# Kernel optimization log

Hardware: AMD Instinct MI355X
Metric: run time of the kernel (lower is better)

## Reference

```python
import jax, jax.numpy as jnp
import numpy as np

N, D, H = 2048, 128, 40


def setup_inputs() -> dict:
    key = jax.random.key(0)
    kx, kw, kv = jax.random.split(key, 3)
    X = jax.random.normal(kx, (N, D), dtype=jnp.float32)
    # nn.Parameter(torch.randn(D, D) / D) per head, stacked over H
    W = jax.random.normal(kw, (H, D, D), dtype=jnp.float32) / D
    V = jax.random.normal(kv, (H, D, D), dtype=jnp.float32) / D
    return {"X": X, "W": W, "V": V}


def reference(X, W, V):
    d = X.shape[1]
    # scores[h] = X @ W[h] @ X.T / sqrt(D)   -> [H, N, N]
    XW = jnp.einsum("nd,hde->hne", X, W)
    scores = jnp.einsum("hne,me->hnm", XW, X) / jnp.sqrt(jnp.asarray(d, X.dtype))
    # softmax over dim=1 of the 2D per-head score matrix == last axis here
    weights = jax.nn.softmax(scores, axis=-1) + 1e-8
    # A[h] = weights[h] @ X @ V[h]; output = sum over heads -> [N, D]
    XV = jnp.einsum("md,hde->hme", X, V)
    out = jnp.einsum("hnm,hme->ne", weights, XV)
    return out
```

## Files before the change

kernel.cpp:

```cpp
#include <hip/hip_runtime.h>
#include <hip/hip_bf16.h>
#include <stdint.h>

#define N 2048
#define D 128
#define H 40

typedef __attribute__((ext_vector_type(8))) short short8;
typedef __attribute__((ext_vector_type(4))) float float4v;
typedef __attribute__((ext_vector_type(8))) float float8v;
typedef __attribute__((ext_vector_type(16))) float float16v;
typedef __attribute__((ext_vector_type(8))) _Float16 half8v;

static __device__ __forceinline__ unsigned short f32_to_bf16(float f) {
  unsigned int u = __builtin_bit_cast(unsigned int, f);
  unsigned int rounding = 0x7FFFu + ((u >> 16) & 1u);
  return (unsigned short)((u + rounding) >> 16);
}

static __device__ __forceinline__ unsigned int pk2(float lo, float hi) {
  return (unsigned int)f32_to_bf16(lo) | ((unsigned int)f32_to_bf16(hi) << 16);
}

static __device__ __forceinline__ unsigned int pk2f(float lo, float hi) {
  unsigned int a = __builtin_bit_cast(unsigned int, lo) + 0x8000u;
  unsigned int b = __builtin_bit_cast(unsigned int, hi) + 0x8000u;
  return __builtin_amdgcn_perm(b, a, 0x07060302u);
}

static __device__ __forceinline__ unsigned long long pack4(float x0, float x1,
                                                           float x2, float x3) {
  return (unsigned long long)pk2(x0, x1) | ((unsigned long long)pk2(x2, x3) << 32);
}

static __device__ __forceinline__ float fast_exp2(float x) {
#if __has_builtin(__builtin_amdgcn_exp2f)
  return __builtin_amdgcn_exp2f(x);
#else
  return __expf(0.69314718056f * x);
#endif
}

static __device__ __forceinline__ void load_lds16(const void* g, void* l) {
  __builtin_amdgcn_global_load_lds(
      (const __attribute__((address_space(1))) unsigned int*)g,
      (__attribute__((address_space(3))) unsigned int*)l, 16, 0, 0);
}

#define MFMA32(a, b, c) __builtin_amdgcn_mfma_f32_32x32x16_bf16((a), (b), (c), 0, 0, 0)

static __device__ __forceinline__ void regs_to_bfrags(const float16v c, int hh,
                                                      short8& f0, short8& f1) {
  unsigned int a0 = pk2f(c[0], c[1]),   a1 = pk2f(c[2], c[3]);
  unsigned int a2 = pk2f(c[4], c[5]),   a3 = pk2f(c[6], c[7]);
  unsigned int a4 = pk2f(c[8], c[9]),   a5 = pk2f(c[10], c[11]);
  unsigned int a6 = pk2f(c[12], c[13]), a7 = pk2f(c[14], c[15]);
  unsigned int x0 = __shfl_xor(hh ? a0 : a2, 32);
  unsigned int x1 = __shfl_xor(hh ? a1 : a3, 32);
  unsigned int x2 = __shfl_xor(hh ? a4 : a6, 32);
  unsigned int x3 = __shfl_xor(hh ? a5 : a7, 32);
  uint4 u0 = {hh ? x0 : a0, hh ? x1 : a1, hh ? a2 : x0, hh ? a3 : x1};
  uint4 u1 = {hh ? x2 : a4, hh ? x3 : a5, hh ? a6 : x2, hh ? a7 : x3};
  f0 = __builtin_bit_cast(short8, u0);
  f1 = __builtin_bit_cast(short8, u1);
}

static __device__ __forceinline__ void regs_to_pfrags(const float16v s, int hh,
                                                      float& lsum, short8& f0,
                                                      short8& f1) {
  float e[16];
  float acc = 0.0f;
#pragma unroll
  for (int i = 0; i < 16; i++) { e[i] = fast_exp2(s[i]); acc += e[i]; }
  lsum += acc;
  unsigned int a0 = pk2f(e[0], e[1]),   a1 = pk2f(e[2], e[3]);
  unsigned int a2 = pk2f(e[4], e[5]),   a3 = pk2f(e[6], e[7]);
  unsigned int a4 = pk2f(e[8], e[9]),   a5 = pk2f(e[10], e[11]);
  unsigned int a6 = pk2f(e[12], e[13]), a7 = pk2f(e[14], e[15]);
  unsigned int x0 = __shfl_xor(hh ? a0 : a2, 32);
  unsigned int x1 = __shfl_xor(hh ? a1 : a3, 32);
  unsigned int x2 = __shfl_xor(hh ? a4 : a6, 32);
  unsigned int x3 = __shfl_xor(hh ? a5 : a7, 32);
  uint4 u0 = {hh ? x0 : a0, hh ? x1 : a1, hh ? a2 : x0, hh ? a3 : x1};
  uint4 u1 = {hh ? x2 : a4, hh ? x3 : a5, hh ? a6 : x2, hh ? a7 : x3};
  f0 = __builtin_bit_cast(short8, u0);
  f1 = __builtin_bit_cast(short8, u1);
}

static __device__ __forceinline__ void stage_64x256(const char* gbase, size_t stride,
                                                    int colOff, char* lds, int wave,
                                                    int lane) {
#pragma unroll
  for (int i = 0; i < 4; i++) {
    int r = wave * 16 + i * 4 + (lane >> 4);
    int us = (lane & 15) ^ (r & 15);
    load_lds16(gbase + (size_t)r * stride + colOff + us * 16,
               lds + (wave * 16 + i * 4) * 256);
  }
}
static __device__ __forceinline__ void stage_128x256(const char* gbase, size_t stride,
                                                     char* lds, int wave, int lane) {
#pragma unroll
  for (int i = 0; i < 8; i++) {
    int r = wave * 32 + i * 4 + (lane >> 4);
    int us = (lane & 15) ^ (r & 15);
    load_lds16(gbase + (size_t)r * stride + us * 16, lds + (wave * 32 + i * 4) * 256);
  }
}
static __device__ __forceinline__ void stage_128x128(const char* gbase, size_t stride,
                                                     int colOff, char* lds, int wave,
                                                     int lane) {
#pragma unroll
  for (int i = 0; i < 4; i++) {
    int m = wave * 16 + i * 4 + (lane >> 4);
    int u = (lane & 15) ^ (m & 15);
    int grow = 2 * m + (u >> 3);
    load_lds16(gbase + (size_t)grow * stride + colOff + (u & 7) * 16,
               lds + (wave * 16 + i * 4) * 256);
  }
}
static __device__ __forceinline__ short8 read_macro(const char* lds, int row, int kunit) {
  int m = row >> 1;
  int u = ((row & 1) << 3) | kunit;
  return *(const short8*)(lds + m * 256 + ((u ^ (m & 15)) * 16));
}

__global__ __launch_bounds__(256)
void xconv_kernel(const float* __restrict__ X, unsigned short* __restrict__ Xb,
                  unsigned short* __restrict__ XbT) {
  const int n0 = blockIdx.x * 128;
  const int tid = threadIdx.x;
  __shared__ __align__(16) unsigned short Lt[128 * 136];
  for (int i = tid; i < 128 * 32; i += 256) {
    int row = i >> 5, c4 = (i & 31) * 4;
    float4v x = *(const float4v*)(X + (size_t)(n0 + row) * D + c4);
    unsigned long long p = pack4(x.x, x.y, x.z, x.w);
    *(unsigned long long*)(Lt + row * 136 + c4) = p;
    *(unsigned long long*)(Xb + (size_t)(n0 + row) * D + c4) = p;
  }
  __syncthreads();
  for (int i = tid; i < 128 * 16; i += 256) {
    int d = i >> 4, g = i & 15;
    short8 v;
#pragma unroll
    for (int j = 0; j < 8; j++) v[j] = (short)Lt[(g * 8 + j) * 136 + d];
    *(short8*)(XbT + (size_t)d * N + n0 + g * 8) = v;
  }
}

__global__ __launch_bounds__(256)
void wvconv_kernel(const float* __restrict__ W, const float* __restrict__ V,
                   unsigned short* __restrict__ Wt, unsigned short* __restrict__ Vt) {
  const int b = blockIdx.x;
  const int mat = (b >= H) ? 1 : 0;
  const int h = mat ? b - H : b;
  const float* src = (mat ? V : W) + (size_t)h * D * D;
  unsigned short* dst = (mat ? Vt : Wt) + (size_t)h * D * D;
  const float scale = mat ? 1.0f : 0.1275174313f;
  const int tid = threadIdx.x;
  __shared__ __align__(16) unsigned short Lt[128 * 136];
  for (int i = tid; i < 128 * 32; i += 256) {
    int d = i >> 5, e4 = (i & 31) * 4;
    float4v w = *(const float4v*)(src + d * D + e4);
    Lt[(e4 + 0) * 136 + d] = f32_to_bf16(w.x * scale);
    Lt[(e4 + 1) * 136 + d] = f32_to_bf16(w.y * scale);
    Lt[(e4 + 2) * 136 + d] = f32_to_bf16(w.z * scale);
    Lt[(e4 + 3) * 136 + d] = f32_to_bf16(w.w * scale);
  }
  __syncthreads();
  for (int i = tid; i < 128 * 16; i += 256) {
    int e = i >> 4, u = i & 15;
    *(uint4*)((char*)dst + (size_t)e * 256 + u * 16) =
        *(const uint4*)((const char*)Lt + (size_t)e * 272 + u * 16);
  }
}

__global__ __launch_bounds__(256)
void attn_kernel(const unsigned short* __restrict__ Xb,
                 const unsigned short* __restrict__ XbT,
                 const unsigned short* __restrict__ Wt,
                 const unsigned short* __restrict__ Vt,
                 unsigned short* __restrict__ Opart, float* __restrict__ Lsum) {
  __shared__ __align__(16) char smem[32768];
  const int bx = blockIdx.x;
  const int kh = bx & 1;
  const int q0 = ((bx >> 1) & 15) << 7;
  const int h = bx >> 5;
  const int tid = threadIdx.x;
  const int wave = tid >> 6, lane = tid & 63;
  const int l = lane & 31, hh = lane >> 5;

  const char* XbB = (const char*)Xb;
  const char* XbTB = (const char*)XbT;
  const char* WtB = (const char*)(Wt + (size_t)h * D * D);
  const char* VtB = (const char*)(Vt + (size_t)h * D * D);

  float16v qa[4];
#pragma unroll
  for (int et = 0; et < 4; et++) qa[et] = (float16v)0.0f;
#pragma unroll
  for (int dh = 0; dh < 2; dh++) {
    __syncthreads();
    stage_128x128(XbB + (size_t)q0 * 256, 256, dh * 128, smem, wave, lane);
    stage_128x128(WtB, 256, dh * 128, smem + 16384, wave, lane);
    __syncthreads();
    short8 xfr[4];
#pragma unroll
    for (int dk = 0; dk < 4; dk++)
      xfr[dk] = read_macro(smem, wave * 32 + l, dk * 2 + hh);
#pragma unroll
    for (int et = 0; et < 4; et++)
#pragma unroll
      for (int dk = 0; dk < 4; dk++) {
        short8 wa = read_macro(smem + 16384, et * 32 + l, dk * 2 + hh);
        qa[et] = MFMA32(wa, xfr[dk], qa[et]);
      }
  }
  short8 qf[8];
#pragma unroll
  for (int et = 0; et < 4; et++)
    regs_to_bfrags(qa[et], hh, qf[2 * et], qf[2 * et + 1]);

  float16v Tacc[4];
#pragma unroll
  for (int dt = 0; dt < 4; dt++) Tacc[dt] = (float16v)0.0f;
  float lsum = 0.0f;

  const int kbase = kh * (N / 2);
  for (int kt = 0; kt < 16; kt++) {
    const int k0 = kbase + kt * 64;
    __syncthreads();
    stage_64x256(XbB + (size_t)k0 * 256, 256, 0, smem, wave, lane);
    stage_128x128(XbTB, 4096, k0 * 2, smem + 16384, wave, lane);
    __syncthreads();
#pragma unroll
    for (int ksub = 0; ksub < 2; ksub++) {
      float16v sa = (float16v)0.0f, sb = (float16v)0.0f;
      const int krow = ksub * 32 + l;
#pragma unroll
      for (int ks = 0; ks < 4; ks++) {
        short8 kfa = *(const short8*)(smem + krow * 256 +
                                      (((2 * ks + hh) ^ (krow & 15)) * 16));
        short8 kfb = *(const short8*)(smem + krow * 256 +
                                      (((2 * (ks + 4) + hh) ^ (krow & 15)) * 16));
        sa = MFMA32(kfa, qf[ks], sa);
        sb = MFMA32(kfb, qf[ks + 4], sb);
      }
      float16v s = sa + sb;
      short8 pf0, pf1;
      regs_to_pfrags(s, hh, lsum, pf0, pf1);
#pragma unroll
      for (int kk = 0; kk < 2; kk++) {
        short8 pf = kk ? pf1 : pf0;
#pragma unroll
        for (int dt = 0; dt < 4; dt++) {
          short8 xt = read_macro(smem + 16384, dt * 32 + l, ksub * 4 + kk * 2 + hh);
          Tacc[dt] = MFMA32(xt, pf, Tacc[dt]);
        }
      }
    }
  }

  float tot = lsum + __shfl_xor(lsum, 32);
  if (hh == 0) Lsum[(size_t)(h * 2 + kh) * N + q0 + wave * 32 + l] = tot;

  short8 tb[8];
#pragma unroll
  for (int dt = 0; dt < 4; dt++)
    regs_to_bfrags(Tacc[dt], hh, tb[2 * dt], tb[2 * dt + 1]);

  __syncthreads();
  stage_128x256(VtB, 256, smem, wave, lane);
  __syncthreads();

  float16v oacc[4];
#pragma unroll
  for (int et = 0; et < 4; et++) oacc[et] = (float16v)0.0f;
#pragma unroll
  for (int et = 0; et < 4; et++) {
    const int erow = et * 32 + l;
#pragma unroll
    for (int dk = 0; dk < 8; dk++) {
      short8 va = *(const short8*)(smem + erow * 256 +
                                   (((2 * dk + hh) ^ (erow & 15)) * 16));
      oacc[et] = MFMA32(va, tb[dk], oacc[et]);
    }
  }

  unsigned short* Oph = Opart + (size_t)(h * 2 + kh) * N * D;
#pragma unroll
  for (int pass = 0; pass < 2; pass++) {
    __syncthreads();
    const int qrow = wave * 32 + l;
#pragma unroll
    for (int etL = 0; etL < 2; etL++) {
      int et = pass * 2 + etL;
#pragma unroll
      for (int g = 0; g < 4; g++) {
        int unit = etL * 8 + 2 * g + hh;
        float4v v;
        v.x = oacc[et][4 * g + 0];
        v.y = oacc[et][4 * g + 1];
        v.z = oacc[et][4 * g + 2];
        v.w = oacc[et][4 * g + 3];
        *(float4v*)(smem + qrow * 256 + ((unit ^ (qrow & 15)) * 16)) = v;
      }
    }
    __syncthreads();
#pragma unroll
    for (int i = 0; i < 8; i++) {
      int idx = i * 256 + tid;
      int qr = idx >> 4, up = idx & 15, u = up ^ (qr & 15);
      float4v v = *(const float4v*)(smem + qr * 256 + up * 16);
      auto h0 = __builtin_amdgcn_cvt_pkrtz(v.x, v.y);
      auto h1 = __builtin_amdgcn_cvt_pkrtz(v.z, v.w);
      uint2 st = {__builtin_bit_cast(unsigned int, h0),
                  __builtin_bit_cast(unsigned int, h1)};
      *(uint2*)(Oph + (size_t)(q0 + qr) * D + pass * 64 + u * 4) = st;
    }
  }
}

__global__ __launch_bounds__(256)
void reduce_kernel(const unsigned short* __restrict__ Opart,
                   const float* __restrict__ Lsum, float* __restrict__ out) {
  int idx = blockIdx.x * 256 + threadIdx.x;
  int n = idx >> 4;
  const uint4* base = (const uint4*)Opart;
  float8v acc = (float8v)0.0f;
#pragma unroll 4
  for (int h = 0; h < H; h++) {
    float lt = Lsum[(size_t)(2 * h) * N + n] + Lsum[(size_t)(2 * h + 1) * N + n];
    float il = __builtin_amdgcn_rcpf(lt);
    uint4 a = base[(size_t)(2 * h) * (N * D / 8) + idx];
    uint4 b = base[(size_t)(2 * h + 1) * (N * D / 8) + idx];
    float8v fa = __builtin_convertvector(__builtin_bit_cast(half8v, a), float8v);
    float8v fb = __builtin_convertvector(__builtin_bit_cast(half8v, b), float8v);
    acc += (fa + fb) * il;
  }
  *(float8v*)(out + (size_t)idx * 8) = acc;
}

extern "C" void kernel_launch(void* const* d_in, const int* in_sizes, int n_in,
                              void* d_out, int out_size, void* d_ws, size_t ws_size,
                              hipStream_t stream) {
  const float* X = (const float*)d_in[0];
  const float* W = (const float*)d_in[1];
  const float* V = (const float*)d_in[2];
  float* out = (float*)d_out;

  unsigned short* Xb = (unsigned short*)d_ws;
  unsigned short* XbT = Xb + (size_t)N * D;
  unsigned short* Wt = XbT + (size_t)N * D;
  unsigned short* Vt = Wt + (size_t)H * D * D;
  unsigned short* Opart = Vt + (size_t)H * D * D;
  float* Lsum = (float*)(Opart + (size_t)H * 2 * N * D);

  xconv_kernel<<<dim3(N / 128), 256, 0, stream>>>(X, Xb, XbT);
  wvconv_kernel<<<dim3(2 * H), 256, 0, stream>>>(W, V, Wt, Vt);
  attn_kernel<<<dim3(16 * 2 * H), 256, 0, stream>>>(Xb, XbT, Wt, Vt, Opart, Lsum);
  reduce_kernel<<<dim3(N * D / 8 / 256), 256, 0, stream>>>(Opart, Lsum, out);
}
```

Baseline: 224.4 us.

## Use FP8 MFMA for scores, double-buffer K tiles, fuse prep kernels

Computes the QK score MFMA in FP8. The query projection is scaled by 64 and X is converted to FP8, and the scale is undone inside exp2. The K/X^T tiles are double-buffered in LDS so the next tile loads while the current one computes, and the V tile staging overlaps the final loop iteration. It also merges the two conversion kernels into one launch, loads the X fragments for the projection directly from global memory, and widens the reduce grid. FP8 scores risk extra precision loss in the softmax, and the larger LDS footprint may reduce occupancy.

```diff
diff --git a/kernel.cpp b/kernel.cpp
--- a/kernel.cpp
+++ b/kernel.cpp
@@ -5,12 +5,12 @@
 #define N 2048
 #define D 128
 #define H 40
+#define NT 16
 
 typedef __attribute__((ext_vector_type(8))) short short8;
 typedef __attribute__((ext_vector_type(4))) float float4v;
-typedef __attribute__((ext_vector_type(8))) float float8v;
 typedef __attribute__((ext_vector_type(16))) float float16v;
-typedef __attribute__((ext_vector_type(8))) _Float16 half8v;
+typedef __attribute__((ext_vector_type(4))) _Float16 half4v;
 
 static __device__ __forceinline__ unsigned short f32_to_bf16(float f) {
   unsigned int u = __builtin_bit_cast(unsigned int, f);
@@ -41,6 +41,15 @@
 #endif
 }
 
+static __device__ __forceinline__ float bf2f(unsigned short u) {
+  unsigned int x = ((unsigned int)u) << 16;
+  return __builtin_bit_cast(float, x);
+}
+
+static __device__ __forceinline__ long long mk64(unsigned int lo, unsigned int hi) {
+  return (long long)(((unsigned long long)hi << 32) | lo);
+}
+
 static __device__ __forceinline__ void load_lds16(const void* g, void* l) {
   __builtin_amdgcn_global_load_lds(
       (const __attribute__((address_space(1))) unsigned int*)g,
@@ -48,6 +57,7 @@
 }
 
 #define MFMA32(a, b, c) __builtin_amdgcn_mfma_f32_32x32x16_bf16((a), (b), (c), 0, 0, 0)
+#define MFMA8(a, b, c) __builtin_amdgcn_mfma_f32_32x32x16_fp8_fp8((a), (b), (c), 0, 0, 0)
 
 static __device__ __forceinline__ void regs_to_bfrags(const float16v c, int hh,
                                                       short8& f0, short8& f1) {
@@ -65,13 +75,30 @@
   f1 = __builtin_bit_cast(short8, u1);
 }
 
+static __device__ __forceinline__ void regs_to_f8frags(const float16v c, int hh,
+                                                       long long& f0, long long& f1) {
+  const float s = 64.0f;
+  int v0 = __builtin_amdgcn_cvt_pk_fp8_f32(c[0] * s, c[1] * s, 0, false);
+  v0 = __builtin_amdgcn_cvt_pk_fp8_f32(c[2] * s, c[3] * s, v0, true);
+  int v1 = __builtin_amdgcn_cvt_pk_fp8_f32(c[4] * s, c[5] * s, 0, false);
+  v1 = __builtin_amdgcn_cvt_pk_fp8_f32(c[6] * s, c[7] * s, v1, true);
+  int v2 = __builtin_amdgcn_cvt_pk_fp8_f32(c[8] * s, c[9] * s, 0, false);
+  v2 = __builtin_amdgcn_cvt_pk_fp8_f32(c[10] * s, c[11] * s, v2, true);
+  int v3 = __builtin_amdgcn_cvt_pk_fp8_f32(c[12] * s, c[13] * s, 0, false);
+  v3 = __builtin_amdgcn_cvt_pk_fp8_f32(c[14] * s, c[15] * s, v3, true);
+  int t0 = __shfl_xor(hh ? v0 : v1, 32);
+  int t1 = __shfl_xor(hh ? v2 : v3, 32);
+  f0 = hh ? mk64((unsigned)t0, (unsigned)v1) : mk64((unsigned)v0, (unsigned)t0);
+  f1 = hh ? mk64((unsigned)t1, (unsigned)v3) : mk64((unsigned)v2, (unsigned)t1);
+}
+
 static __device__ __forceinline__ void regs_to_pfrags(const float16v s, int hh,
                                                       float& lsum, short8& f0,
                                                       short8& f1) {
   float e[16];
   float acc = 0.0f;
 #pragma unroll
-  for (int i = 0; i < 16; i++) { e[i] = fast_exp2(s[i]); acc += e[i]; }
+  for (int i = 0; i < 16; i++) { e[i] = fast_exp2(s[i] * 0.015625f); acc += e[i]; }
   lsum += acc;
   unsigned int a0 = pk2f(e[0], e[1]),   a1 = pk2f(e[2], e[3]);
   unsigned int a2 = pk2f(e[4], e[5]),   a3 = pk2f(e[6], e[7]);
@@ -119,6 +146,17 @@
                lds + (wave * 16 + i * 4) * 256);
   }
 }
+static __device__ __forceinline__ void stage_k8(const char* gbase, char* lds,
+                                                int wave, int lane) {
+#pragma unroll
+  for (int i = 0; i < 2; i++) {
+    int m = wave * 8 + i * 4 + (lane >> 4);
+    int u = (lane & 15) ^ (m & 15);
+    int grow = 2 * m + (u >> 3);
+    load_lds16(gbase + (size_t)grow * 128 + (u & 7) * 16,
+               lds + (wave * 8 + i * 4) * 256);
+  }
+}
 static __device__ __forceinline__ short8 read_macro(const char* lds, int row, int kunit) {
   int m = row >> 1;
   int u = ((row & 1) << 3) | kunit;
@@ -126,62 +164,82 @@
 }
 
 __global__ __launch_bounds__(256)
-void xconv_kernel(const float* __restrict__ X, unsigned short* __restrict__ Xb,
-                  unsigned short* __restrict__ XbT) {
-  const int n0 = blockIdx.x * 128;
+void prep_kernel(const float* __restrict__ X, const float* __restrict__ W,
+                 const float* __restrict__ V, unsigned short* __restrict__ Xb,
+                 unsigned short* __restrict__ XbT, unsigned char* __restrict__ Xf8,
+                 unsigned short* __restrict__ Wt, unsigned short* __restrict__ Vt) {
   const int tid = threadIdx.x;
   __shared__ __align__(16) unsigned short Lt[128 * 136];
-  for (int i = tid; i < 128 * 32; i += 256) {
-    int row = i >> 5, c4 = (i & 31) * 4;
-    float4v x = *(const float4v*)(X + (size_t)(n0 + row) * D + c4);
-    unsigned long long p = pack4(x.x, x.y, x.z, x.w);
-    *(unsigned long long*)(Lt + row * 136 + c4) = p;
-    *(unsigned long long*)(Xb + (size_t)(n0 + row) * D + c4) = p;
-  }
-  __syncthreads();
-  for (int i = tid; i < 128 * 16; i += 256) {
-    int d = i >> 4, g = i & 15;
-    short8 v;
-#pragma unroll
-    for (int j = 0; j < 8; j++) v[j] = (short)Lt[(g * 8 + j) * 136 + d];
-    *(short8*)(XbT + (size_t)d * N + n0 + g * 8) = v;
-  }
-}
-
-__global__ __launch_bounds__(256)
-void wvconv_kernel(const float* __restrict__ W, const float* __restrict__ V,
-                   unsigned short* __restrict__ Wt, unsigned short* __restrict__ Vt) {
-  const int b = blockIdx.x;
-  const int mat = (b >= H) ? 1 : 0;
-  const int h = mat ? b - H : b;
-  const float* src = (mat ? V : W) + (size_t)h * D * D;
-  unsigned short* dst = (mat ? Vt : Wt) + (size_t)h * D * D;
-  const float scale = mat ? 1.0f : 0.1275174313f;
-  const int tid = threadIdx.x;
-  __shared__ __align__(16) unsigned short Lt[128 * 136];
-  for (int i = tid; i < 128 * 32; i += 256) {
-    int d = i >> 5, e4 = (i & 31) * 4;
-    float4v w = *(const float4v*)(src + d * D + e4);
-    Lt[(e4 + 0) * 136 + d] = f32_to_bf16(w.x * scale);
-    Lt[(e4 + 1) * 136 + d] = f32_to_bf16(w.y * scale);
-    Lt[(e4 + 2) * 136 + d] = f32_to_bf16(w.z * scale);
-    Lt[(e4 + 3) * 136 + d] = f32_to_bf16(w.w * scale);
-  }
-  __syncthreads();
-  for (int i = tid; i < 128 * 16; i += 256) {
-    int e = i >> 4, u = i & 15;
-    *(uint4*)((char*)dst + (size_t)e * 256 + u * 16) =
-        *(const uint4*)((const char*)Lt + (size_t)e * 272 + u * 16);
+  if (blockIdx.x < 16) {
+    const int n0 = blockIdx.x * 128;
+    for (int i = tid; i < 128 * 32; i += 256) {
+      int row = i >> 5, c4 = (i & 31) * 4;
+      float4v x = *(const float4v*)(X + (size_t)(n0 + row) * D + c4);
+      unsigned long long p = pack4(x.x, x.y, x.z, x.w);
+      *(unsigned long long*)(Lt + row * 136 + c4) = p;
+      *(unsigned long long*)(Xb + (size_t)(n0 + row) * D + c4) = p;
+    }
+    __syncthreads();
+    for (int i = tid; i < 128 * 16; i += 256) {
+      int d = i >> 4, g = i & 15;
+      short8 v;
+#pragma unroll
+      for (int j = 0; j < 8; j++) v[j] = (short)Lt[(g * 8 + j) * 136 + d];
+      *(short8*)(XbT + (size_t)d * N + n0 + g * 8) = v;
+    }
+    for (int i = tid; i < 128 * 8; i += 256) {
+      int row = i >> 3, c = i & 7, t = c >> 1, o8 = (c & 1) * 8;
+      const unsigned short* lp = Lt + row * 136;
+      int d0 = t * 32 + o8, d1 = t * 32 + 16 + o8;
+      short8 xa = *(const short8*)(lp + d0);
+      short8 xb = *(const short8*)(lp + d1);
+      int w0 = __builtin_amdgcn_cvt_pk_fp8_f32(bf2f(xa[0]), bf2f(xa[1]), 0, false);
+      w0 = __builtin_amdgcn_cvt_pk_fp8_f32(bf2f(xa[2]), bf2f(xa[3]), w0, true);
+      int w1 = __builtin_amdgcn_cvt_pk_fp8_f32(bf2f(xa[4]), bf2f(xa[5]), 0, false);
+      w1 = __builtin_amdgcn_cvt_pk_fp8_f32(bf2f(xa[6]), bf2f(xa[7]), w1, true);
+      int w2 = __builtin_amdgcn_cvt_pk_fp8_f32(bf2f(xb[0]), bf2f(xb[1]), 0, false);
+      w2 = __builtin_amdgcn_cvt_pk_fp8_f32(bf2f(xb[2]), bf2f(xb[3]), w2, true);
+      int w3 = __builtin_amdgcn_cvt_pk_fp8_f32(bf2f(xb[4]), bf2f(xb[5]), 0, false);
+      w3 = __builtin_amdgcn_cvt_pk_fp8_f32(bf2f(xb[6]), bf2f(xb[7]), w3, true);
+      uint4 st = {(unsigned)w0, (unsigned)w1, (unsigned)w2, (unsigned)w3};
+      *(uint4*)(Xf8 + (size_t)(n0 + row) * 128 + c * 16) = st;
+    }
+  } else {
+    const int b = blockIdx.x - 16;
+    const int mat = (b >= H) ? 1 : 0;
+    const int h = mat ? b - H : b;
+    const float* src = (mat ? V : W) + (size_t)h * D * D;
+    unsigned short* dst = (mat ? Vt : Wt) + (size_t)h * D * D;
+    const float scale = mat ? 1.0f : 0.1275174313f;
+    for (int i = tid; i < 128 * 32; i += 256) {
+      int d = i >> 5, e4 = (i & 31) * 4;
+      float4v w = *(const float4v*)(src + d * D + e4);
+      Lt[(e4 + 0) * 136 + d] = f32_to_bf16(w.x * scale);
+      Lt[(e4 + 1) * 136 + d] = f32_to_bf16(w.y * scale);
+      Lt[(e4 + 2) * 136 + d] = f32_to_bf16(w.z * scale);
+      Lt[(e4 + 3) * 136 + d] = f32_to_bf16(w.w * scale);
+    }
+    __syncthreads();
+    for (int i = tid; i < 128 * 16; i += 256) {
+      int e = i >> 4, u = i & 15;
+      *(uint4*)((char*)dst + (size_t)e * 256 + u * 16) =
+          *(const uint4*)((const char*)Lt + (size_t)e * 272 + u * 16);
+    }
   }
 }
 
 __global__ __launch_bounds__(256)
 void attn_kernel(const unsigned short* __restrict__ Xb,
+                 const unsigned char* __restrict__ Xf8,
                  const unsigned short* __restrict__ XbT,
                  const unsigned short* __restrict__ Wt,
                  const unsigned short* __restrict__ Vt,
                  unsigned short* __restrict__ Opart, float* __restrict__ Lsum) {
-  __shared__ __align__(16) char smem[32768];
+  __shared__ __align__(16) char smem[49152];
+  char* XA = smem;
+  char* XB = smem + 16384;
+  char* KA = smem + 32768;
+  char* KB = smem + 40960;
   const int bx = blockIdx.x;
   const int kh = bx & 1;
   const int q0 = ((bx >> 1) & 15) << 7;
@@ -191,62 +249,71 @@
   const int l = lane & 31, hh = lane >> 5;
 
   const char* XbB = (const char*)Xb;
+  const char* Xf8B = (const char*)Xf8;
   const char* XbTB = (const char*)XbT;
   const char* WtB = (const char*)(Wt + (size_t)h * D * D);
   const char* VtB = (const char*)(Vt + (size_t)h * D * D);
+  const int kbase = kh * (N / 2);
+
+  stage_128x256(WtB, 256, smem, wave, lane);
+  stage_k8(Xf8B + (size_t)kbase * 128, KA, wave, lane);
+  short8 xfr[8];
+#pragma unroll
+  for (int dk = 0; dk < 8; dk++)
+    xfr[dk] = *(const short8*)(XbB + (size_t)(q0 + wave * 32 + l) * 256 + dk * 32 + hh * 16);
+  __syncthreads();
 
   float16v qa[4];
 #pragma unroll
   for (int et = 0; et < 4; et++) qa[et] = (float16v)0.0f;
 #pragma unroll
-  for (int dh = 0; dh < 2; dh++) {
-    __syncthreads();
-    stage_128x128(XbB + (size_t)q0 * 256, 256, dh * 128, smem, wave, lane);
-    stage_128x128(WtB, 256, dh * 128, smem + 16384, wave, lane);
-    __syncthreads();
-    short8 xfr[4];
-#pragma unroll
-    for (int dk = 0; dk < 4; dk++)
-      xfr[dk] = read_macro(smem, wave * 32 + l, dk * 2 + hh);
-#pragma unroll
-    for (int et = 0; et < 4; et++)
-#pragma unroll
-      for (int dk = 0; dk < 4; dk++) {
-        short8 wa = read_macro(smem + 16384, et * 32 + l, dk * 2 + hh);
-        qa[et] = MFMA32(wa, xfr[dk], qa[et]);
-      }
-  }
-  short8 qf[8];
+  for (int et = 0; et < 4; et++) {
+    const int r = et * 32 + l;
+#pragma unroll
+    for (int dk = 0; dk < 8; dk++) {
+      short8 wa = *(const short8*)(smem + r * 256 + (((2 * dk + hh) ^ (r & 15)) * 16));
+      qa[et] = MFMA32(wa, xfr[dk], qa[et]);
+    }
+  }
+  long long qf8[8];
 #pragma unroll
   for (int et = 0; et < 4; et++)
-    regs_to_bfrags(qa[et], hh, qf[2 * et], qf[2 * et + 1]);
+    regs_to_f8frags(qa[et], hh, qf8[2 * et], qf8[2 * et + 1]);
 
   float16v Tacc[4];
 #pragma unroll
   for (int dt = 0; dt < 4; dt++) Tacc[dt] = (float16v)0.0f;
   float lsum = 0.0f;
-
-  const int kbase = kh * (N / 2);
-  for (int kt = 0; kt < 16; kt++) {
-    const int k0 = kbase + kt * 64;
-    __syncthreads();
-    stage_64x256(XbB + (size_t)k0 * 256, 256, 0, smem, wave, lane);
-    stage_128x128(XbTB, 4096, k0 * 2, smem + 16384, wave, lane);
-    __syncthreads();
+  __syncthreads();
+
+  stage_128x128(XbTB, 4096, kbase * 2, XA, wave, lane);
+  __syncthreads();
+
+  for (int kt = 0; kt < NT; kt++) {
+    const char* curK = (kt & 1) ? KB : KA;
+    const char* curX = (kt & 1) ? XB : XA;
+    char* altK = (kt & 1) ? KA : KB;
+    char* altX = (kt & 1) ? XA : XB;
+    if (kt + 1 < NT) {
+      const int k0n = kbase + (kt + 1) * 64;
+      stage_k8(Xf8B + (size_t)k0n * 128, altK, wave, lane);
+      stage_128x128(XbTB, 4096, k0n * 2, altX, wave, lane);
+    } else {
+      stage_64x256(VtB, 256, 0, altX, wave, lane);
+    }
 #pragma unroll
     for (int ksub = 0; ksub < 2; ksub++) {
-      float16v sa = (float16v)0.0f, sb = (float16v)0.0f;
+      float16v s = (float16v)0.0f;
       const int krow = ksub * 32 + l;
-#pragma unroll
-      for (int ks = 0; ks < 4; ks++) {
-        short8 kfa = *(const short8*)(smem + krow * 256 +
-                                      (((2 * ks + hh) ^ (krow & 15)) * 16));
-        short8 kfb = *(const short8*)(smem + krow * 256 +
-                                      (((2 * (ks + 4) + hh) ^ (krow & 15)) * 16));
-        sa = MFMA32(kfa, qf[ks], sa);
-        sb = MFMA32(kfb, qf[ks + 4], sb);
+      const int mb = (krow >> 1) * 256, m16 = (krow >> 1) & 15;
+      const int rsel = (krow & 1) << 3;
+#pragma unroll
+      for (int t = 0; t < 4; t++) {
+        int u = (rsel | (t * 2 + hh)) ^ m16;
+        uint4 w = *(const uint4*)(curK + mb + u * 16);
+        s = MFMA8(mk64(w.x, w.y), qf8[2 * t], s);
+        s = MFMA8(mk64(w.z, w.w), qf8[2 * t + 1], s);
       }
-      float16v s = sa + sb;
       short8 pf0, pf1;
       regs_to_pfrags(s, hh, lsum, pf0, pf1);
 #pragma unroll
@@ -254,35 +321,42 @@
         short8 pf = kk ? pf1 : pf0;
 #pragma unroll
         for (int dt = 0; dt < 4; dt++) {
-          short8 xt = read_macro(smem + 16384, dt * 32 + l, ksub * 4 + kk * 2 + hh);
+          short8 xt = read_macro(curX, dt * 32 + l, ksub * 4 + kk * 2 + hh);
           Tacc[dt] = MFMA32(xt, pf, Tacc[dt]);
         }
       }
     }
+    __syncthreads();
   }
 
   float tot = lsum + __shfl_xor(lsum, 32);
   if (hh == 0) Lsum[(size_t)(h * 2 + kh) * N + q0 + wave * 32 + l] = tot;
 
+  stage_64x256(VtB + 64 * 256, 256, 0, XB, wave, lane);
   short8 tb[8];
 #pragma unroll
   for (int dt = 0; dt < 4; dt++)
     regs_to_bfrags(Tacc[dt], hh, tb[2 * dt], tb[2 * dt + 1]);
 
+  float16v oacc[4];
+#pragma unroll
+  for (int et = 0; et < 4; et++) oacc[et] = (float16v)0.0f;
+#pragma unroll
+  for (int et = 0; et < 2; et++) {
+    const int r = et * 32 + l;
+#pragma unroll
+    for (int dk = 0; dk < 8; dk++) {
+      short8 va = *(const short8*)(XA + r * 256 + (((2 * dk + hh) ^ (r & 15)) * 16));
+      oacc[et] = MFMA32(va, tb[dk], oacc[et]);
+    }
+  }
   __syncthreads();
-  stage_128x256(VtB, 256, smem, wave, lane);
-  __syncthreads();
-
-  float16v oacc[4];
-#pragma unroll
-  for (int et = 0; et < 4; et++) oacc[et] = (float16v)0.0f;
-#pragma unroll
-  for (int et = 0; et < 4; et++) {
-    const int erow = et * 32 + l;
+#pragma unroll
+  for (int et = 2; et < 4; et++) {
+    const int r = (et - 2) * 32 + l;
 #pragma unroll
     for (int dk = 0; dk < 8; dk++) {
-      short8 va = *(const short8*)(smem + erow * 256 +
-                                   (((2 * dk + hh) ^ (erow & 15)) * 16));
+      short8 va = *(const short8*)(XB + r * 256 + (((2 * dk + hh) ^ (r & 15)) * 16));
       oacc[et] = MFMA32(va, tb[dk], oacc[et]);
     }
   }
@@ -325,20 +399,20 @@
 void reduce_kernel(const unsigned short* __restrict__ Opart,
                    const float* __restrict__ Lsum, float* __restrict__ out) {
   int idx = blockIdx.x * 256 + threadIdx.x;
-  int n = idx >> 4;
-  const uint4* base = (const uint4*)Opart;
-  float8v acc = (float8v)0.0f;
-#pragma unroll 4
+  int n = idx >> 5;
+  const uint2* base = (const uint2*)Opart;
+  float4v acc = (float4v)0.0f;
+#pragma unroll 8
   for (int h = 0; h < H; h++) {
     float lt = Lsum[(size_t)(2 * h) * N + n] + Lsum[(size_t)(2 * h + 1) * N + n];
     float il = __builtin_amdgcn_rcpf(lt);
-    uint4 a = base[(size_t)(2 * h) * (N * D / 8) + idx];
-    uint4 b = base[(size_t)(2 * h + 1) * (N * D / 8) + idx];
-    float8v fa = __builtin_convertvector(__builtin_bit_cast(half8v, a), float8v);
-    float8v fb = __builtin_convertvector(__builtin_bit_cast(half8v, b), float8v);
+    uint2 a = base[(size_t)(2 * h) * (N * D / 4) + idx];
+    uint2 b = base[(size_t)(2 * h + 1) * (N * D / 4) + idx];
+    float4v fa = __builtin_convertvector(__builtin_bit_cast(half4v, a), float4v);
+    float4v fb = __builtin_convertvector(__builtin_bit_cast(half4v, b), float4v);
     acc += (fa + fb) * il;
   }
-  *(float8v*)(out + (size_t)idx * 8) = acc;
+  *(float4v*)(out + (size_t)idx * 4) = acc;
 }
 
 extern "C" void kernel_launch(void* const* d_in, const int* in_sizes, int n_in,
@@ -353,11 +427,11 @@
   unsigned short* XbT = Xb + (size_t)N * D;
   unsigned short* Wt = XbT + (size_t)N * D;
   unsigned short* Vt = Wt + (size_t)H * D * D;
-  unsigned short* Opart = Vt + (size_t)H * D * D;
+  unsigned char* Xf8 = (unsigned char*)(Vt + (size_t)H * D * D);
+  unsigned short* Opart = (unsigned short*)(Xf8 + (size_t)N * D);
   float* Lsum = (float*)(Opart + (size_t)H * 2 * N * D);
 
-  xconv_kernel<<<dim3(N / 128), 256, 0, stream>>>(X, Xb, XbT);
-  wvconv_kernel<<<dim3(2 * H), 256, 0, stream>>>(W, V, Wt, Vt);
-  attn_kernel<<<dim3(16 * 2 * H), 256, 0, stream>>>(Xb, XbT, Wt, Vt, Opart, Lsum);
-  reduce_kernel<<<dim3(N * D / 8 / 256), 256, 0, stream>>>(Opart, Lsum, out);
-}
+  prep_kernel<<<dim3(16 + 2 * H), 256, 0, stream>>>(X, W, V, Xb, XbT, Xf8, Wt, Vt);
+  attn_kernel<<<dim3(NT * 2 * H), 256, 0, stream>>>(Xb, Xf8, XbT, Wt, Vt, Opart, Lsum);
+  reduce_kernel<<<dim3(N * D / 4 / 256), 256, 0, stream>>>(Opart, Lsum, out);
+}
```

Measured after the change: 191.3 us. 1.17x faster.
